# Optimization experiments

Measured on AMD Instinct MI355X. Metric: run time of the kernel, lower is better.

Reference implementation:

```python
import jax, jax.numpy as jnp
import numpy as np

# Cost coefficients from MatcherConfig (init_kwargs)
C_CLASS, C_MASK, C_DICE, C_DIST, C_NLL, C_LIK = 2.0, 5.0, 5.0, 1.0, 0.5, 0.5

B, P, Q, E = 8, 16384, 256, 128  # images, pixels (H*W), queries, electrons


def setup_inputs() -> dict:
    key = jax.random.key(0)
    ks = jax.random.split(key, 8)
    mask_mask = jax.random.uniform(ks[0], (B, P, Q)) < 0.10           # sparsity pattern of pred logits
    mask_logit_values = jax.random.normal(ks[1], (B, P, Q), jnp.float32)
    seg_occ = jax.random.uniform(ks[2], (B, P, E)) < 0.05              # sparsity pattern of target segmap
    seg_vals = jax.random.uniform(ks[3], (B, P, E), jnp.float32, 1e-3, 1.0)
    segmap_values = jnp.where(seg_occ, seg_vals, 0.0)
    pred_logits = jax.random.normal(ks[4], (B, Q), jnp.float32)
    pred_positions = jax.random.uniform(ks[5], (B, Q, 2), jnp.float32)
    true_positions = jax.random.uniform(ks[6], (B, E, 2), jnp.float32)
    kd, ko = jax.random.split(ks[7])
    diag = 1.0 + 2.0 * jax.random.uniform(kd, (B, Q, 2), jnp.float32)  # positive diag of scale_tril
    off = 0.3 * jax.random.normal(ko, (B, Q), jnp.float32)
    pred_chol = jnp.zeros((B, Q, 2, 2), jnp.float32)
    pred_chol = pred_chol.at[..., 0, 0].set(diag[..., 0])
    pred_chol = pred_chol.at[..., 1, 1].set(diag[..., 1])
    pred_chol = pred_chol.at[..., 1, 0].set(off)
    image_sizes_xy = jnp.full((B, 2), 128.0, jnp.float32)
    return {
        'pred_logits': pred_logits,
        'mask_logit_values': mask_logit_values,
        'mask_mask': mask_mask,
        'segmap_values': segmap_values,
        'pred_positions': pred_positions,
        'pred_chol': pred_chol,
        'true_positions': true_positions,
        'image_sizes_xy': image_sizes_xy,
    }


def _total_cost(pred_logits, mask_logit_values, segmap_values, pred_positions,
                pred_chol, true_positions, image_sizes_xy, mask_mask):
    sp = jax.nn.softplus
    m = mask_mask
    # --- class cost: BCE(logit, 1) per query -> [B,Q]
    class_cost = sp(-pred_logits)
    # --- mask BCE cost (get_bce_cost): sparse entries only
    pos = jnp.where(m, sp(-mask_logit_values), 0.0)   # BCE vs 1 on nnz entries
    neg = jnp.where(m, sp(mask_logit_values), 0.0)    # BCE vs 0 on nnz entries
    targ = (segmap_values > 0).astype(pos.dtype)      # binarized target segmap
    pos_loss = jnp.einsum('bpq,bpe->bqe', pos, targ)
    neg_loss = neg.sum(1)[:, :, None] - jnp.einsum('bpq,bpe->bqe', neg, targ)
    nnz = jnp.maximum(targ.sum((1, 2)), 1.0)          # target _nnz() per image
    mask_cost = (pos_loss + neg_loss) / nnz[:, None, None]
    # --- dice cost (get_dice_cost): sparse softmax over query dim
    NEG = jnp.asarray(-1e30, mask_logit_values.dtype)
    z = jnp.where(m, mask_logit_values, NEG)
    mx = jnp.max(z, axis=-1, keepdims=True)
    ez = jnp.where(m, jnp.exp(z - mx), 0.0)
    s = ez.sum(-1, keepdims=True)
    pred_p = jnp.where(s > 0, ez / jnp.maximum(s, 1e-30), 0.0)  # [B,P,Q]
    num = 2.0 * jnp.einsum('bpq,bpe->bqe', pred_p, segmap_values)
    den = pred_p.sum(1)[:, :, None] + segmap_values.sum(1)[:, None, :]
    dice_cost = 1.0 - (num + 1.0) / (den + 1.0)
    # --- huber distance cost (delta=1), mean over xy
    d = pred_positions[:, :, None, :] - true_positions[:, None, :, :]  # [B,Q,E,2]
    ad = jnp.abs(d)
    huber_cost = jnp.where(ad < 1.0, 0.5 * d * d, ad - 0.5).mean(-1)
    # --- NLL / likelihood distance costs (MVN with scale_tril)
    mu = pred_positions * image_sizes_xy[:, None, :]
    y = true_positions * image_sizes_xy[:, None, :]
    diff = y[:, None, :, :] - mu[:, :, None, :]        # [B,Q,E,2]
    L00 = pred_chol[..., 0, 0][:, :, None]
    L10 = pred_chol[..., 1, 0][:, :, None]
    L11 = pred_chol[..., 1, 1][:, :, None]
    z0 = diff[..., 0] / L00
    z1 = (diff[..., 1] - L10 * z0) / L11
    nll_cost = 0.5 * (z0 * z0 + z1 * z1) + jnp.log(2.0 * jnp.pi) + jnp.log(L00) + jnp.log(L11)
    lik_cost = 1.0 - jnp.exp(-nll_cost)
    total = (C_CLASS * class_cost[:, :, None] + C_MASK * mask_cost + C_DICE * dice_cost
             + C_DIST * huber_cost + C_NLL * nll_cost + C_LIK * lik_cost)
    return total  # [B, Q, E] stacked per-image cost matrices


def reference(pred_logits, mask_logit_values, mask_mask, segmap_values,
              pred_positions, pred_chol, true_positions, image_sizes_xy):
    return _total_cost(pred_logits, mask_logit_values, segmap_values, pred_positions,
                       pred_chol, true_positions, image_sizes_xy, mask_mask)
```

## Files before the change

### kernel.cpp

```cpp
#include <hip/hip_runtime.h>
#include <cstdint>
#include <cstddef>

typedef float v4f __attribute__((ext_vector_type(4)));
typedef short short8 __attribute__((ext_vector_type(8)));

constexpr int B_ = 8, P_ = 16384, Q_ = 256, E_ = 128;

__device__ __forceinline__ unsigned int f2bf(float f) {
  unsigned int x = __float_as_uint(f);
  x += 0x7FFFu + ((x >> 16) & 1u);
  return x >> 16;
}
__device__ __forceinline__ float softplus_f(float x) {
  return fmaxf(x, 0.f) + __logf(1.f + __expf(-fabsf(x)));
}
__device__ __forceinline__ float wsum(float v) {
#pragma unroll
  for (int o = 32; o; o >>= 1) v += __shfl_xor(v, o, 64);
  return v;
}
__device__ __forceinline__ void lds_barrier() {
  asm volatile("s_waitcnt lgkmcnt(0)" ::: "memory");
  __builtin_amdgcn_s_barrier();
}
__device__ __forceinline__ int swz(int q, int kp) {
  return ((q << 4) | kp) ^ (((q >> 3) & 7) << 2);
}

template<bool DIRECT>
__global__ __launch_bounds__(512, 2) void fused_all(
    const float* __restrict__ mlv, const int* __restrict__ mask,
    const float* __restrict__ seg, float* __restrict__ part,
    float* __restrict__ negsum, float* __restrict__ ppsum,
    float* __restrict__ segsum, float* __restrict__ nnzb)
{
  __shared__ __align__(16) unsigned int lds[12288];
  unsigned int* A1q = lds;
  unsigned int* EZq = lds + 4096;
  unsigned int* SBq = lds + 8192;
  unsigned int* STq = lds + 10240;

  const int t = threadIdx.x, w = t >> 6, l = t & 63;
  const int lm = l & 15, quad = l >> 4;
  const int wr = w & 3, wc = w >> 2;
  const int jj = l >> 5, le = l & 31;
  const int b = blockIdx.x >> 5, ks = blockIdx.x & 31;

  v4f acc0[4][4], acc1[4][4];
#pragma unroll
  for (int i = 0; i < 4; ++i)
#pragma unroll
    for (int j = 0; j < 4; ++j) { acc0[i][j] = (v4f)0.f; acc1[i][j] = (v4f)0.f; }
  float accN[4] = {0.f,0.f,0.f,0.f};
  float accP[4] = {0.f,0.f,0.f,0.f};
  float accS[4] = {0.f,0.f,0.f,0.f};
  float cnt = 0.f;

  const float* mp = mlv + ((size_t)b * P_ + ks * 512 + 4 * w) * Q_ + 4 * l;
  const int*   kp = mask + ((size_t)b * P_ + ks * 512 + 4 * w) * Q_ + 4 * l;
  const float* sp = seg + ((size_t)b * P_ + ks * 512 + 4 * w + 2 * jj) * E_ + 4 * le;

  float4 X[4]; int4 M[4]; float4 S0, S1;
#pragma unroll
  for (int r = 0; r < 4; ++r) {
    X[r] = *(const float4*)(mp + (size_t)r * Q_);
    M[r] = *(const int4*)(kp + (size_t)r * Q_);
  }
  S0 = *(const float4*)(sp);
  S1 = *(const float4*)(sp + E_);

  for (int it = 0; it < 16; ++it) {
    float xs[4][4]; int ms[4][4];
#pragma unroll
    for (int r = 0; r < 4; ++r) {
      xs[r][0] = X[r].x; xs[r][1] = X[r].y; xs[r][2] = X[r].z; xs[r][3] = X[r].w;
      ms[r][0] = M[r].x; ms[r][1] = M[r].y; ms[r][2] = M[r].z; ms[r][3] = M[r].w;
    }
    float sv0[4] = {S0.x, S0.y, S0.z, S0.w};
    float sv1[4] = {S1.x, S1.y, S1.z, S1.w};

    if (it < 15) {
      mp += 32 * Q_; kp += 32 * Q_; sp += 32 * E_;
#pragma unroll
      for (int r = 0; r < 4; ++r) {
        X[r] = *(const float4*)(mp + (size_t)r * Q_);
        M[r] = *(const int4*)(kp + (size_t)r * Q_);
      }
      S0 = *(const float4*)(sp);
      S1 = *(const float4*)(sp + E_);
    }

    float ez[4][4], rs[4];
#pragma unroll
    for (int r = 0; r < 4; ++r) {
      float s = 0.f;
#pragma unroll
      for (int j = 0; j < 4; ++j) {
        const bool mm = ms[r][j] != 0;
        const float e = mm ? __expf(xs[r][j]) : 0.f;
        ez[r][j] = e; s += e;
        accN[j] += __logf(1.f + e);
      }
      rs[r] = s;
    }
#pragma unroll
    for (int r = 0; r < 4; ++r) rs[r] = wsum(rs[r]);
    float inv[4];
#pragma unroll
    for (int r = 0; r < 4; ++r) inv[r] = (rs[r] > 0.f) ? (1.f / rs[r]) : 0.f;

    unsigned int a1p[2][4], ezp[2][4];
#pragma unroll
    for (int jp = 0; jp < 2; ++jp)
#pragma unroll
      for (int j = 0; j < 4; ++j) {
        const int r0 = 2 * jp, r1 = 2 * jp + 1;
        a1p[jp][j] = f2bf(ms[r0][j] ? -xs[r0][j] : 0.f)
                   | (f2bf(ms[r1][j] ? -xs[r1][j] : 0.f) << 16);
        const float p0 = ez[r0][j] * inv[r0];
        const float p1 = ez[r1][j] * inv[r1];
        accP[j] += p0 + p1;
        ezp[jp][j] = f2bf(p0) | (f2bf(p1) << 16);
      }
    unsigned int sb[4], st_[4];
#pragma unroll
    for (int j = 0; j < 4; ++j) {
      accS[j] += sv0[j] + sv1[j];
      cnt += ((sv0[j] > 0.f) ? 1.f : 0.f) + ((sv1[j] > 0.f) ? 1.f : 0.f);
      sb[j]  = ((sv0[j] > 0.f) ? 0x3F80u : 0u) | ((sv1[j] > 0.f) ? 0x3F800000u : 0u);
      st_[j] = f2bf(sv0[j]) | (f2bf(sv1[j]) << 16);
    }

    lds_barrier();
#pragma unroll
    for (int j = 0; j < 4; ++j) {
      const int q = 4 * l + j;
      const int wa = swz(q, 2 * w);
      uint2 va; va.x = a1p[0][j]; va.y = a1p[1][j];
      uint2 ve; ve.x = ezp[0][j]; ve.y = ezp[1][j];
      *(uint2*)(A1q + wa) = va;
      *(uint2*)(EZq + wa) = ve;
    }
#pragma unroll
    for (int j = 0; j < 4; ++j) {
      const int e = 4 * le + j;
      const int wb = swz(e, 2 * w + jj);
      SBq[wb] = sb[j];
      STq[wb] = st_[j];
    }
    lds_barrier();

    short8 af0[4], af1[4], bf0[4], bf1[4];
#pragma unroll
    for (int i = 0; i < 4; ++i) {
      const int q_abs = wr * 64 + i * 16 + lm;
      const int wa = swz(q_abs, 4 * quad);
      af0[i] = *(const short8*)(A1q + wa);
      af1[i] = *(const short8*)(EZq + wa);
    }
#pragma unroll
    for (int j = 0; j < 4; ++j) {
      const int e_abs = wc * 64 + j * 16 + lm;
      const int wb = swz(e_abs, 4 * quad);
      bf0[j] = *(const short8*)(SBq + wb);
      bf1[j] = *(const short8*)(STq + wb);
    }
#pragma unroll
    for (int i = 0; i < 4; ++i)
#pragma unroll
      for (int j = 0; j < 4; ++j) {
        acc0[i][j] = __builtin_amdgcn_mfma_f32_16x16x32_bf16(af0[i], bf0[j], acc0[i][j], 0, 0, 0);
        acc1[i][j] = __builtin_amdgcn_mfma_f32_16x16x32_bf16(af1[i], bf1[j], acc1[i][j], 0, 0, 0);
      }
  }

  __syncthreads();
  float* fr = (float*)lds;
#pragma unroll
  for (int j = 0; j < 4; ++j) {
    fr[w * 256 + 4 * l + j] = accN[j];
    fr[2048 + w * 256 + 4 * l + j] = accP[j];
    fr[4096 + (2 * w + jj) * 128 + 4 * le + j] = accS[j];
  }
  __syncthreads();
  if (t < 256) {
    float sn = 0.f, sq = 0.f;
#pragma unroll
    for (int k = 0; k < 8; ++k) { sn += fr[k * 256 + t]; sq += fr[2048 + k * 256 + t]; }
    atomicAdd(&negsum[b * 256 + t], sn);
    atomicAdd(&ppsum[b * 256 + t], sq);
  } else if (t < 384) {
    const int e = t - 256;
    float ss = 0.f;
#pragma unroll
    for (int k = 0; k < 16; ++k) ss += fr[4096 + k * 128 + e];
    atomicAdd(&segsum[b * 128 + e], ss);
  }
  cnt = wsum(cnt);
  if (l == 0) atomicAdd(&nnzb[b], cnt);

  if constexpr (DIRECT) {
    float* p0 = part + ((size_t)(ks * 8 + b) * 2) * 32768;
    float* p1 = p0 + 32768;
#pragma unroll
    for (int i = 0; i < 4; ++i)
#pragma unroll
      for (int r = 0; r < 4; ++r) {
        const int q = wr * 64 + i * 16 + quad * 4 + r;
#pragma unroll
        for (int j = 0; j < 4; ++j) {
          const int e = wc * 64 + j * 16 + lm;
          p0[q * 128 + e] = acc0[i][j][r];
          p1[q * 128 + e] = acc1[i][j][r];
        }
      }
  } else {
    float* p0 = part + (size_t)b * 32768;
    float* p1 = part + (size_t)(8 + b) * 32768;
#pragma unroll
    for (int i = 0; i < 4; ++i)
#pragma unroll
      for (int r = 0; r < 4; ++r) {
        const int q = wr * 64 + i * 16 + quad * 4 + r;
#pragma unroll
        for (int j = 0; j < 4; ++j) {
          const int e = wc * 64 + j * 16 + lm;
          atomicAdd(&p0[q * 128 + e], acc0[i][j][r]);
          atomicAdd(&p1[q * 128 + e], acc1[i][j][r]);
        }
      }
  }
}

template<bool DIRECT>
__global__ __launch_bounds__(128) void epilogue(
    const float* __restrict__ part,
    const float* __restrict__ negsum, const float* __restrict__ ppsum,
    const float* __restrict__ segsum, const float* __restrict__ nnzb,
    const float* __restrict__ logits, const float* __restrict__ ppos,
    const float* __restrict__ chol, const float* __restrict__ tpos,
    const float* __restrict__ imgsz, float* __restrict__ out)
{
  const int bq = blockIdx.x;
  const int b = bq >> 8;
  const int e = threadIdx.x;
  const int qe = (bq & 255) * 128 + e;

  float g1, g2;
  if constexpr (DIRECT) {
    g1 = 0.f; g2 = 0.f;
#pragma unroll 8
    for (int ksi = 0; ksi < 32; ++ksi) {
      g1 += part[((size_t)(ksi * 8 + b) * 2) * 32768 + qe];
      g2 += part[((size_t)(ksi * 8 + b) * 2 + 1) * 32768 + qe];
    }
  } else {
    g1 = part[(size_t)b * 32768 + qe];
    g2 = part[(size_t)(8 + b) * 32768 + qe];
  }

  const float nnz = fmaxf(nnzb[b], 1.f);
  const float mask_cost = (negsum[bq] + g1) / nnz;
  const float dice = 1.f - (2.f * g2 + 1.f) / (ppsum[bq] + segsum[b * 128 + e] + 1.f);
  const float cls = softplus_f(-logits[bq]);
  const float px = ppos[bq * 2], py = ppos[bq * 2 + 1];
  const float tx = tpos[(b * 128 + e) * 2], ty = tpos[(b * 128 + e) * 2 + 1];
  const float dx = px - tx, dy = py - ty;
  const float ax = fabsf(dx), ay = fabsf(dy);
  const float hx = (ax < 1.f) ? 0.5f * dx * dx : ax - 0.5f;
  const float hy = (ay < 1.f) ? 0.5f * dy * dy : ay - 0.5f;
  const float huber = 0.5f * (hx + hy);
  const float sx = imgsz[b * 2], sy = imgsz[b * 2 + 1];
  const float L00 = chol[bq * 4 + 0], L10 = chol[bq * 4 + 2], L11 = chol[bq * 4 + 3];
  const float d0 = (tx - px) * sx, d1 = (ty - py) * sy;
  const float z0 = d0 / L00;
  const float z1 = (d1 - L10 * z0) / L11;
  const float nll = 0.5f * (z0 * z0 + z1 * z1) + 1.8378770664093453f + __logf(L00) + __logf(L11);
  const float lik = 1.f - __expf(-nll);
  out[bq * 128 + e] = 2.f * cls + 5.f * mask_cost + 5.f * dice + huber + 0.5f * nll + 0.5f * lik;
}

extern "C" void kernel_launch(void* const* d_in, const int* in_sizes, int n_in,
                              void* d_out, int out_size, void* d_ws, size_t ws_size,
                              hipStream_t stream)
{
  (void)in_sizes; (void)n_in; (void)out_size;
  const float* logits = (const float*)d_in[0];
  const float* mlv    = (const float*)d_in[1];
  const int*   mask   = (const int*)d_in[2];
  const float* seg    = (const float*)d_in[3];
  const float* ppos   = (const float*)d_in[4];
  const float* chol   = (const float*)d_in[5];
  const float* tpos   = (const float*)d_in[6];
  const float* imgsz  = (const float*)d_in[7];

  char* ws = (char*)d_ws;
  const size_t PART_DIRECT = 67108864ull;
  const size_t NEED = PART_DIRECT + 20512ull;

  if (ws_size >= NEED) {
    float* part   = (float*)ws;
    float* negsum = (float*)(ws + PART_DIRECT);
    float* ppsum  = (float*)(ws + PART_DIRECT + 8192);
    float* segsum = (float*)(ws + PART_DIRECT + 16384);
    float* nnzb   = (float*)(ws + PART_DIRECT + 20480);
    hipMemsetAsync(ws + PART_DIRECT, 0, 20512, stream);
    fused_all<true><<<256, 512, 0, stream>>>(mlv, mask, seg, part, negsum, ppsum, segsum, nnzb);
    epilogue<true><<<2048, 128, 0, stream>>>(part, negsum, ppsum, segsum, nnzb,
                                             logits, ppos, chol, tpos, imgsz, (float*)d_out);
  } else {
    float* part   = (float*)(ws);
    float* negsum = (float*)(ws + 2097152);
    float* ppsum  = (float*)(ws + 2105344);
    float* segsum = (float*)(ws + 2113536);
    float* nnzb   = (float*)(ws + 2117632);
    hipMemsetAsync(ws, 0, 2117664, stream);
    fused_all<false><<<256, 512, 0, stream>>>(mlv, mask, seg, part, negsum, ppsum, segsum, nnzb);
    epilogue<false><<<2048, 128, 0, stream>>>(part, negsum, ppsum, segsum, nnzb,
                                              logits, ppos, chol, tpos, imgsz, (float*)d_out);
  }
}
```

Measured before the change: 421.0 us.

## Use 1024-thread blocks with double-buffered LDS and half-K MFMA fragments

Doubles the block to 16 waves, each processing one pixel row per iteration with scalar loads, and double-buffers the LDS staging tiles so only one barrier per iteration is needed. The K dimension per MFMA is halved: fragments for the upper quads read a shared zero region, so each wave covers 64x32 outputs with padded-K MFMAs. The intent is more latency hiding and fewer barriers. The cost is wasted MFMA work on zero padding, scalar rather than vector global loads, and 16-bit LDS stores that may conflict.

```diff
diff --git a/kernel.cpp b/kernel.cpp
--- a/kernel.cpp
+++ b/kernel.cpp
@@ -24,177 +24,135 @@
   asm volatile("s_waitcnt lgkmcnt(0)" ::: "memory");
   __builtin_amdgcn_s_barrier();
 }
-__device__ __forceinline__ int swz(int q, int kp) {
-  return ((q << 4) | kp) ^ (((q >> 3) & 7) << 2);
+
+#define ZW 15360
+__device__ __forceinline__ short8 ldfrag(const unsigned int* lds, int rowbase, int quad) {
+  const int a = (quad < 2) ? (rowbase + 4 * quad) : ZW;
+  union { unsigned int u[4]; short8 s; } x;
+  *(uint2*)(x.u)     = *(const uint2*)(lds + a);
+  *(uint2*)(x.u + 2) = *(const uint2*)(lds + a + 2);
+  return x.s;
 }
 
 template<bool DIRECT>
-__global__ __launch_bounds__(512, 2) void fused_all(
+__global__ __launch_bounds__(1024) void fused_all(
     const float* __restrict__ mlv, const int* __restrict__ mask,
     const float* __restrict__ seg, float* __restrict__ part,
     float* __restrict__ negsum, float* __restrict__ ppsum,
     float* __restrict__ segsum, float* __restrict__ nnzb)
 {
-  __shared__ __align__(16) unsigned int lds[12288];
-  unsigned int* A1q = lds;
-  unsigned int* EZq = lds + 4096;
-  unsigned int* SBq = lds + 8192;
-  unsigned int* STq = lds + 10240;
+  __shared__ __align__(16) unsigned int lds[15376];
 
   const int t = threadIdx.x, w = t >> 6, l = t & 63;
   const int lm = l & 15, quad = l >> 4;
   const int wr = w & 3, wc = w >> 2;
-  const int jj = l >> 5, le = l & 31;
+  const int kw = w >> 1, kh = w & 1;
   const int b = blockIdx.x >> 5, ks = blockIdx.x & 31;
 
-  v4f acc0[4][4], acc1[4][4];
+  if (t < 4) lds[ZW + t] = 0u;
+
+  v4f acc0[4][2], acc1[4][2];
 #pragma unroll
   for (int i = 0; i < 4; ++i)
 #pragma unroll
-    for (int j = 0; j < 4; ++j) { acc0[i][j] = (v4f)0.f; acc1[i][j] = (v4f)0.f; }
+    for (int j = 0; j < 2; ++j) { acc0[i][j] = (v4f)0.f; acc1[i][j] = (v4f)0.f; }
   float accN[4] = {0.f,0.f,0.f,0.f};
   float accP[4] = {0.f,0.f,0.f,0.f};
-  float accS[4] = {0.f,0.f,0.f,0.f};
+  float accS[2] = {0.f,0.f};
   float cnt = 0.f;
 
-  const float* mp = mlv + ((size_t)b * P_ + ks * 512 + 4 * w) * Q_ + 4 * l;
-  const int*   kp = mask + ((size_t)b * P_ + ks * 512 + 4 * w) * Q_ + 4 * l;
-  const float* sp = seg + ((size_t)b * P_ + ks * 512 + 4 * w + 2 * jj) * E_ + 4 * le;
-
-  float4 X[4]; int4 M[4]; float4 S0, S1;
-#pragma unroll
-  for (int r = 0; r < 4; ++r) {
-    X[r] = *(const float4*)(mp + (size_t)r * Q_);
-    M[r] = *(const int4*)(kp + (size_t)r * Q_);
-  }
-  S0 = *(const float4*)(sp);
-  S1 = *(const float4*)(sp + E_);
-
-  for (int it = 0; it < 16; ++it) {
-    float xs[4][4]; int ms[4][4];
-#pragma unroll
-    for (int r = 0; r < 4; ++r) {
-      xs[r][0] = X[r].x; xs[r][1] = X[r].y; xs[r][2] = X[r].z; xs[r][3] = X[r].w;
-      ms[r][0] = M[r].x; ms[r][1] = M[r].y; ms[r][2] = M[r].z; ms[r][3] = M[r].w;
-    }
-    float sv0[4] = {S0.x, S0.y, S0.z, S0.w};
-    float sv1[4] = {S1.x, S1.y, S1.z, S1.w};
-
-    if (it < 15) {
-      mp += 32 * Q_; kp += 32 * Q_; sp += 32 * E_;
-#pragma unroll
-      for (int r = 0; r < 4; ++r) {
-        X[r] = *(const float4*)(mp + (size_t)r * Q_);
-        M[r] = *(const int4*)(kp + (size_t)r * Q_);
+  const float* mp = mlv + ((size_t)b * P_ + ks * 512 + w) * Q_ + l;
+  const int*   kp = mask + ((size_t)b * P_ + ks * 512 + w) * Q_ + l;
+  const float* sp = seg + ((size_t)b * P_ + ks * 512 + w) * E_ + l;
+
+  float X[4]; int M[4]; float S[2];
+#pragma unroll
+  for (int j = 0; j < 4; ++j) { X[j] = mp[64 * j]; M[j] = kp[64 * j]; }
+  S[0] = sp[0]; S[1] = sp[64];
+
+  for (int it = 0; it < 32; ++it) {
+    const int bb = (it & 1) * 7680;
+
+    float xs[4]; int ms[4]; float sv[2];
+#pragma unroll
+    for (int j = 0; j < 4; ++j) { xs[j] = X[j]; ms[j] = M[j]; }
+    sv[0] = S[0]; sv[1] = S[1];
+
+    if (it < 31) {
+      mp += 16 * Q_; kp += 16 * Q_; sp += 16 * E_;
+#pragma unroll
+      for (int j = 0; j < 4; ++j) { X[j] = mp[64 * j]; M[j] = kp[64 * j]; }
+      S[0] = sp[0]; S[1] = sp[64];
+    }
+
+    float ez[4], s = 0.f;
+#pragma unroll
+    for (int j = 0; j < 4; ++j) {
+      const float e = ms[j] ? __expf(xs[j]) : 0.f;
+      ez[j] = e; s += e;
+      accN[j] += __logf(1.f + e);
+    }
+    s = wsum(s);
+    const float inv = (s > 0.f) ? (1.f / s) : 0.f;
+
+    unsigned short* hs = (unsigned short*)lds;
+#pragma unroll
+    for (int j = 0; j < 4; ++j) {
+      const int q = l + 64 * j;
+      const float p = ez[j] * inv;
+      accP[j] += p;
+      hs[(bb + q * 10 + kw) * 2 + kh]        = (unsigned short)f2bf(ms[j] ? -xs[j] : 0.f);
+      hs[(bb + 2560 + q * 10 + kw) * 2 + kh] = (unsigned short)f2bf(p);
+    }
+#pragma unroll
+    for (int jj = 0; jj < 2; ++jj) {
+      const int e = l + 64 * jj;
+      accS[jj] += sv[jj];
+      cnt += (sv[jj] > 0.f) ? 1.f : 0.f;
+      hs[(bb + 5120 + e * 10 + kw) * 2 + kh] = (sv[jj] > 0.f) ? (unsigned short)0x3F80 : (unsigned short)0;
+      hs[(bb + 6400 + e * 10 + kw) * 2 + kh] = (unsigned short)f2bf(sv[jj]);
+    }
+
+    lds_barrier();
+
+#pragma unroll
+    for (int j2 = 0; j2 < 2; ++j2) {
+      const int eb = wc * 32 + j2 * 16 + lm;
+      const short8 bf0 = ldfrag(lds, bb + 5120 + eb * 10, quad);
+      const short8 bf1 = ldfrag(lds, bb + 6400 + eb * 10, quad);
+#pragma unroll
+      for (int i = 0; i < 4; ++i) {
+        const int qa = wr * 64 + i * 16 + lm;
+        const short8 af0 = ldfrag(lds, bb + qa * 10, quad);
+        const short8 af1 = ldfrag(lds, bb + 2560 + qa * 10, quad);
+        acc0[i][j2] = __builtin_amdgcn_mfma_f32_16x16x32_bf16(af0, bf0, acc0[i][j2], 0, 0, 0);
+        acc1[i][j2] = __builtin_amdgcn_mfma_f32_16x16x32_bf16(af1, bf1, acc1[i][j2], 0, 0, 0);
       }
-      S0 = *(const float4*)(sp);
-      S1 = *(const float4*)(sp + E_);
-    }
-
-    float ez[4][4], rs[4];
-#pragma unroll
-    for (int r = 0; r < 4; ++r) {
-      float s = 0.f;
-#pragma unroll
-      for (int j = 0; j < 4; ++j) {
-        const bool mm = ms[r][j] != 0;
-        const float e = mm ? __expf(xs[r][j]) : 0.f;
-        ez[r][j] = e; s += e;
-        accN[j] += __logf(1.f + e);
-      }
-      rs[r] = s;
-    }
-#pragma unroll
-    for (int r = 0; r < 4; ++r) rs[r] = wsum(rs[r]);
-    float inv[4];
-#pragma unroll
-    for (int r = 0; r < 4; ++r) inv[r] = (rs[r] > 0.f) ? (1.f / rs[r]) : 0.f;
-
-    unsigned int a1p[2][4], ezp[2][4];
-#pragma unroll
-    for (int jp = 0; jp < 2; ++jp)
-#pragma unroll
-      for (int j = 0; j < 4; ++j) {
-        const int r0 = 2 * jp, r1 = 2 * jp + 1;
-        a1p[jp][j] = f2bf(ms[r0][j] ? -xs[r0][j] : 0.f)
-                   | (f2bf(ms[r1][j] ? -xs[r1][j] : 0.f) << 16);
-        const float p0 = ez[r0][j] * inv[r0];
-        const float p1 = ez[r1][j] * inv[r1];
-        accP[j] += p0 + p1;
-        ezp[jp][j] = f2bf(p0) | (f2bf(p1) << 16);
-      }
-    unsigned int sb[4], st_[4];
-#pragma unroll
-    for (int j = 0; j < 4; ++j) {
-      accS[j] += sv0[j] + sv1[j];
-      cnt += ((sv0[j] > 0.f) ? 1.f : 0.f) + ((sv1[j] > 0.f) ? 1.f : 0.f);
-      sb[j]  = ((sv0[j] > 0.f) ? 0x3F80u : 0u) | ((sv1[j] > 0.f) ? 0x3F800000u : 0u);
-      st_[j] = f2bf(sv0[j]) | (f2bf(sv1[j]) << 16);
-    }
-
-    lds_barrier();
-#pragma unroll
-    for (int j = 0; j < 4; ++j) {
-      const int q = 4 * l + j;
-      const int wa = swz(q, 2 * w);
-      uint2 va; va.x = a1p[0][j]; va.y = a1p[1][j];
-      uint2 ve; ve.x = ezp[0][j]; ve.y = ezp[1][j];
-      *(uint2*)(A1q + wa) = va;
-      *(uint2*)(EZq + wa) = ve;
-    }
-#pragma unroll
-    for (int j = 0; j < 4; ++j) {
-      const int e = 4 * le + j;
-      const int wb = swz(e, 2 * w + jj);
-      SBq[wb] = sb[j];
-      STq[wb] = st_[j];
-    }
-    lds_barrier();
-
-    short8 af0[4], af1[4], bf0[4], bf1[4];
-#pragma unroll
-    for (int i = 0; i < 4; ++i) {
-      const int q_abs = wr * 64 + i * 16 + lm;
-      const int wa = swz(q_abs, 4 * quad);
-      af0[i] = *(const short8*)(A1q + wa);
-      af1[i] = *(const short8*)(EZq + wa);
-    }
-#pragma unroll
-    for (int j = 0; j < 4; ++j) {
-      const int e_abs = wc * 64 + j * 16 + lm;
-      const int wb = swz(e_abs, 4 * quad);
-      bf0[j] = *(const short8*)(SBq + wb);
-      bf1[j] = *(const short8*)(STq + wb);
-    }
-#pragma unroll
-    for (int i = 0; i < 4; ++i)
-#pragma unroll
-      for (int j = 0; j < 4; ++j) {
-        acc0[i][j] = __builtin_amdgcn_mfma_f32_16x16x32_bf16(af0[i], bf0[j], acc0[i][j], 0, 0, 0);
-        acc1[i][j] = __builtin_amdgcn_mfma_f32_16x16x32_bf16(af1[i], bf1[j], acc1[i][j], 0, 0, 0);
-      }
+    }
   }
 
   __syncthreads();
   float* fr = (float*)lds;
 #pragma unroll
   for (int j = 0; j < 4; ++j) {
-    fr[w * 256 + 4 * l + j] = accN[j];
-    fr[2048 + w * 256 + 4 * l + j] = accP[j];
-    fr[4096 + (2 * w + jj) * 128 + 4 * le + j] = accS[j];
-  }
+    fr[w * 256 + l + 64 * j] = accN[j];
+    fr[4096 + w * 256 + l + 64 * j] = accP[j];
+  }
+#pragma unroll
+  for (int jj = 0; jj < 2; ++jj)
+    fr[8192 + w * 128 + l + 64 * jj] = accS[jj];
   __syncthreads();
   if (t < 256) {
     float sn = 0.f, sq = 0.f;
 #pragma unroll
-    for (int k = 0; k < 8; ++k) { sn += fr[k * 256 + t]; sq += fr[2048 + k * 256 + t]; }
+    for (int k = 0; k < 16; ++k) { sn += fr[k * 256 + t]; sq += fr[4096 + k * 256 + t]; }
     atomicAdd(&negsum[b * 256 + t], sn);
     atomicAdd(&ppsum[b * 256 + t], sq);
   } else if (t < 384) {
     const int e = t - 256;
     float ss = 0.f;
 #pragma unroll
-    for (int k = 0; k < 16; ++k) ss += fr[4096 + k * 128 + e];
+    for (int k = 0; k < 16; ++k) ss += fr[8192 + k * 128 + e];
     atomicAdd(&segsum[b * 128 + e], ss);
   }
   cnt = wsum(cnt);
@@ -209,10 +167,10 @@
       for (int r = 0; r < 4; ++r) {
         const int q = wr * 64 + i * 16 + quad * 4 + r;
 #pragma unroll
-        for (int j = 0; j < 4; ++j) {
-          const int e = wc * 64 + j * 16 + lm;
-          p0[q * 128 + e] = acc0[i][j][r];
-          p1[q * 128 + e] = acc1[i][j][r];
+        for (int j2 = 0; j2 < 2; ++j2) {
+          const int e = wc * 32 + j2 * 16 + lm;
+          p0[q * 128 + e] = acc0[i][j2][r];
+          p1[q * 128 + e] = acc1[i][j2][r];
         }
       }
   } else {
@@ -224,10 +182,10 @@
       for (int r = 0; r < 4; ++r) {
         const int q = wr * 64 + i * 16 + quad * 4 + r;
 #pragma unroll
-        for (int j = 0; j < 4; ++j) {
-          const int e = wc * 64 + j * 16 + lm;
-          atomicAdd(&p0[q * 128 + e], acc0[i][j][r]);
-          atomicAdd(&p1[q * 128 + e], acc1[i][j][r]);
+        for (int j2 = 0; j2 < 2; ++j2) {
+          const int e = wc * 32 + j2 * 16 + lm;
+          atomicAdd(&p0[q * 128 + e], acc0[i][j2][r]);
+          atomicAdd(&p1[q * 128 + e], acc1[i][j2][r]);
         }
       }
   }
@@ -306,7 +264,7 @@
     float* segsum = (float*)(ws + PART_DIRECT + 16384);
     float* nnzb   = (float*)(ws + PART_DIRECT + 20480);
     hipMemsetAsync(ws + PART_DIRECT, 0, 20512, stream);
-    fused_all<true><<<256, 512, 0, stream>>>(mlv, mask, seg, part, negsum, ppsum, segsum, nnzb);
+    fused_all<true><<<256, 1024, 0, stream>>>(mlv, mask, seg, part, negsum, ppsum, segsum, nnzb);
     epilogue<true><<<2048, 128, 0, stream>>>(part, negsum, ppsum, segsum, nnzb,
                                              logits, ppos, chol, tpos, imgsz, (float*)d_out);
   } else {
@@ -316,7 +274,7 @@
     float* segsum = (float*)(ws + 2113536);
     float* nnzb   = (float*)(ws + 2117632);
     hipMemsetAsync(ws, 0, 2117664, stream);
-    fused_all<false><<<256, 512, 0, stream>>>(mlv, mask, seg, part, negsum, ppsum, segsum, nnzb);
+    fused_all<false><<<256, 1024, 0, stream>>>(mlv, mask, seg, part, negsum, ppsum, segsum, nnzb);
     epilogue<false><<<2048, 128, 0, stream>>>(part, negsum, ppsum, segsum, nnzb,
                                               logits, ppos, chol, tpos, imgsz, (float*)d_out);
   }
```

Result: slower. 457.0 us (+8.6%).
